# Kernel tuning notes

Hardware: AMD Instinct MI355X
Metric: run time of the kernel (lower is better)

Reference implementation:

```python
import jax, jax.numpy as jnp
import numpy as np

N_EMBD = 1024
N_HEAD = 16
HEAD_SIZE = N_EMBD // N_HEAD


def setup_inputs() -> dict:
    key = jax.random.key(0)
    k1, k2, k3, k4 = jax.random.split(key, 4)
    x = jax.random.normal(k1, (2, 2048, N_EMBD), dtype=jnp.float32)
    # nn.Linear weights: stored as [out, in]; apply as x @ W.T
    scale = 1.0 / np.sqrt(N_EMBD)
    W_kqv = jax.random.uniform(k2, (3 * N_EMBD, N_EMBD), jnp.float32, -scale, scale)
    W_proj = jax.random.uniform(k3, (N_EMBD, N_EMBD), jnp.float32, -scale, scale)
    b_proj = jax.random.uniform(k4, (N_EMBD,), jnp.float32, -scale, scale)
    return {"x": x, "W_kqv": W_kqv, "W_proj": W_proj, "b_proj": b_proj}


def reference(x, W_kqv, W_proj, b_proj):
    B, T, C = x.shape
    H, D = N_HEAD, HEAD_SIZE
    kqv = x @ W_kqv.T  # [B, T, 3C]
    # source splits as k, q, v (k first)
    k, q, v = jnp.split(kqv, 3, axis=-1)
    k = k.reshape(B, T, H, D).transpose(0, 2, 1, 3)  # [B,H,T,D]
    q = q.reshape(B, T, H, D).transpose(0, 2, 1, 3)
    v = v.reshape(B, T, H, D).transpose(0, 2, 1, 3)
    wei = jnp.einsum('bhqd,bhkd->bhqk', q, k) * (D ** -0.5)  # [B,H,T,T]
    causal = jnp.tril(jnp.ones((T, T), dtype=bool))
    wei = jnp.where(causal[None, None], wei, -jnp.inf)
    wei = jax.nn.softmax(wei, axis=-1)
    out = jnp.einsum('bhqk,bhkd->bhqd', wei, v)  # [B,H,T,D]
    out = out.transpose(0, 2, 1, 3).reshape(B, T, C)
    return out @ W_proj.T + b_proj
```

## Files before the change

### kernel.cpp

```cpp
#include <hip/hip_runtime.h>
#include <cstdint>


typedef __bf16 bf16x8 __attribute__((ext_vector_type(8)));
typedef unsigned short u16x8 __attribute__((ext_vector_type(8)));
typedef float f32x4 __attribute__((ext_vector_type(4)));

__device__ __forceinline__ float bf2f(unsigned short u) {
    return __uint_as_float(((unsigned int)u) << 16);
}
__device__ __forceinline__ unsigned short f2bf(float f) {
    unsigned int u = __float_as_uint(f);
    u += 0x7fffu + ((u >> 16) & 1u);
    return (unsigned short)(u >> 16);
}
__device__ __forceinline__ void stC(float* p, float v) { *p = v; }
__device__ __forceinline__ void stC(unsigned short* p, float v) { *p = f2bf(v); }

__device__ __forceinline__ void gl2lds16(const unsigned short* g, unsigned short* l) {
    __builtin_amdgcn_global_load_lds(
        (__attribute__((address_space(1))) void*)g,
        (__attribute__((address_space(3))) void*)l, 16, 0, 0);
}

__device__ __forceinline__ unsigned short* swz(unsigned short* base, int row, int col) {
    const int off = ((row << 7) + (col << 1)) ^ ((row & 7) << 4);
    return (unsigned short*)((char*)base + off);
}
__device__ __forceinline__ const unsigned short* swz(const unsigned short* base, int row, int col) {
    const int off = ((row << 7) + (col << 1)) ^ ((row & 7) << 4);
    return (const unsigned short*)((const char*)base + off);
}

__device__ __forceinline__ void cvt8(const float* __restrict__ s, unsigned short* __restrict__ d) {
    const f32x4 a = *(const f32x4*)s;
    const f32x4 b = *(const f32x4*)(s + 4);
    u16x8 o;
    o[0] = f2bf(a[0]); o[1] = f2bf(a[1]); o[2] = f2bf(a[2]); o[3] = f2bf(a[3]);
    o[4] = f2bf(b[0]); o[5] = f2bf(b[1]); o[6] = f2bf(b[2]); o[7] = f2bf(b[3]);
    *(u16x8*)d = o;
}
__global__ __launch_bounds__(256) void cvt_bf16_3(
    const float* __restrict__ s0, unsigned short* __restrict__ d0, int n0,
    const float* __restrict__ s1, unsigned short* __restrict__ d1, int n1,
    const float* __restrict__ s2, unsigned short* __restrict__ d2, int n2)
{
    const int t = blockIdx.x * 256 + threadIdx.x;
    const int S = gridDim.x * 256;
    for (int i = t; i < n0 / 8; i += S) cvt8(s0 + (size_t)i * 8, d0 + (size_t)i * 8);
    for (int i = t; i < n1 / 8; i += S) cvt8(s1 + (size_t)i * 8, d1 + (size_t)i * 8);
    for (int i = t; i < n2 / 8; i += S) cvt8(s2 + (size_t)i * 8, d2 + (size_t)i * 8);
}

__global__ __launch_bounds__(256, 3) void gemm_qkv(
    const unsigned short* __restrict__ A, const unsigned short* __restrict__ B,
    unsigned short* __restrict__ C, int M, int N, int K)
{
    __shared__ __align__(16) unsigned short As[128 * 32];
    __shared__ __align__(16) unsigned short Bs[128 * 32];

    const int tid = threadIdx.x;
    const int bn = blockIdx.x, bm = blockIdx.y;
    const int w = tid >> 6, lane = tid & 63;
    const int quad = lane >> 4, l16 = lane & 15;
    const int wm = (w >> 1) * 64, wn = (w & 1) * 64;

    f32x4 acc[4][4] = {};

    const int srow = w * 16 + (lane >> 2);
    const int scol = (lane & 3) * 8;
    const unsigned short* Ag = &A[(size_t)(bm * 128 + srow) * K + scol];
    const unsigned short* Bg = &B[(size_t)(bn * 128 + srow) * K + scol];
    unsigned short* AsW = &As[(w * 16) * 32];
    unsigned short* BsW = &Bs[(w * 16) * 32];

    for (int k0 = 0; k0 < K; k0 += 32) {
        gl2lds16(Ag + k0, AsW);
        gl2lds16(Ag + (size_t)64 * K + k0, AsW + 64 * 32);
        gl2lds16(Bg + k0, BsW);
        gl2lds16(Bg + (size_t)64 * K + k0, BsW + 64 * 32);
        __syncthreads();

        bf16x8 af[4], bfr[4];
#pragma unroll
        for (int t = 0; t < 4; t++) {
            af[t]  = *(const bf16x8*)&As[(wm + t * 16 + l16) * 32 + quad * 8];
            bfr[t] = *(const bf16x8*)&Bs[(wn + t * 16 + l16) * 32 + quad * 8];
        }
#pragma unroll
        for (int mt = 0; mt < 4; mt++)
#pragma unroll
            for (int nt = 0; nt < 4; nt++)
                acc[mt][nt] = __builtin_amdgcn_mfma_f32_16x16x32_bf16(
                    af[mt], bfr[nt], acc[mt][nt], 0, 0, 0);
        __syncthreads();
    }

#pragma unroll
    for (int mt = 0; mt < 4; mt++) {
        const int row = bm * 128 + wm + mt * 16 + quad * 4;
#pragma unroll
        for (int nt = 0; nt < 4; nt++) {
            const int col = bn * 128 + wn + nt * 16 + l16;
#pragma unroll
            for (int r = 0; r < 4; r++)
                stC(&C[(size_t)(row + r) * N + col], acc[mt][nt][r]);
        }
    }
}

__global__ __launch_bounds__(256) void gemm_proj(
    const unsigned short* __restrict__ A, const unsigned short* __restrict__ B,
    const float* __restrict__ bias, float* __restrict__ C, int M, int N, int K)
{
    __shared__ __align__(16) unsigned short As[64 * 32];
    __shared__ __align__(16) unsigned short Bs[128 * 32];

    const int tid = threadIdx.x;
    const int bn = blockIdx.x, bm = blockIdx.y;
    const int w = tid >> 6, lane = tid & 63;
    const int quad = lane >> 4, l16 = lane & 15;
    const int wm = (w >> 1) * 32, wn = (w & 1) * 64;

    f32x4 acc[2][4] = {};

    const int srow = w * 16 + (lane >> 2);
    const int scol = (lane & 3) * 8;
    const unsigned short* Ag = &A[(size_t)(bm * 64 + srow) * K + scol];
    const unsigned short* Bg = &B[(size_t)(bn * 128 + srow) * K + scol];
    unsigned short* AsW = &As[(w * 16) * 32];
    unsigned short* BsW = &Bs[(w * 16) * 32];

    for (int k0 = 0; k0 < K; k0 += 32) {
        gl2lds16(Ag + k0, AsW);
        gl2lds16(Bg + k0, BsW);
        gl2lds16(Bg + (size_t)64 * K + k0, BsW + 64 * 32);
        __syncthreads();

        bf16x8 af[2], bfr[4];
#pragma unroll
        for (int t = 0; t < 2; t++)
            af[t]  = *(const bf16x8*)&As[(wm + t * 16 + l16) * 32 + quad * 8];
#pragma unroll
        for (int t = 0; t < 4; t++)
            bfr[t] = *(const bf16x8*)&Bs[(wn + t * 16 + l16) * 32 + quad * 8];
#pragma unroll
        for (int mt = 0; mt < 2; mt++)
#pragma unroll
            for (int nt = 0; nt < 4; nt++)
                acc[mt][nt] = __builtin_amdgcn_mfma_f32_16x16x32_bf16(
                    af[mt], bfr[nt], acc[mt][nt], 0, 0, 0);
        __syncthreads();
    }

#pragma unroll
    for (int mt = 0; mt < 2; mt++) {
        const int row = bm * 64 + wm + mt * 16 + quad * 4;
#pragma unroll
        for (int nt = 0; nt < 4; nt++) {
            const int col = bn * 128 + wn + nt * 16 + l16;
            const float bv = bias[col];
#pragma unroll
            for (int r = 0; r < 4; r++)
                C[(size_t)(row + r) * N + col] = acc[mt][nt][r] + bv;
        }
    }
}

__global__ __launch_bounds__(256) void attn_fused(
    const unsigned short* __restrict__ kqv,
    unsigned short* __restrict__ out)
{
    __shared__ __align__(16) unsigned short Ks[2][64 * 64];
    __shared__ __align__(16) unsigned short Vts[2][64 * 64];
    __shared__ __align__(16) unsigned short Ps[64 * 64];

    const int bh = blockIdx.x;
    const int qt = 31 - (int)blockIdx.y;
    const int b = bh >> 4, h = bh & 15;
    const int tid = threadIdx.x;
    const int w = tid >> 6;
    const int lane = tid & 63;
    const int quad = lane >> 4, l16 = lane & 15;
    const int rowBase = b * 2048;
    const int kOff = h * 64, qOff = 1024 + h * 64, vOff = 2048 + h * 64;
    const float SEXP = 0.125f * 1.4426950408889634f;
    const float MASKV = -1.0e30f;

    bf16x8 aq[2];
    {
        const size_t qrow = (size_t)(rowBase + qt * 64 + w * 16 + l16) * 3072 + qOff;
        aq[0] = *(const bf16x8*)&kqv[qrow + quad * 8];
        aq[1] = *(const bf16x8*)&kqv[qrow + 32 + quad * 8];
    }

    f32x4 o[4] = {};
    float l_i[4] = {0.f, 0.f, 0.f, 0.f};

    u16x8 kr[2], vr[2];
#pragma unroll
    for (int i = 0; i < 2; i++) {
        const int v = tid + i * 256;
        kr[i] = *(const u16x8*)&kqv[(size_t)(rowBase + (v >> 3)) * 3072 + kOff + (v & 7) * 8];
        vr[i] = *(const u16x8*)&kqv[(size_t)(rowBase + lane) * 3072 + vOff + (i * 4 + w) * 8];
    }

    for (int j = 0; j <= qt; j++) {
        const int cur = j & 1;
#pragma unroll
        for (int i = 0; i < 2; i++) {
            const int v = tid + i * 256;
            *(u16x8*)swz(Ks[cur], v >> 3, (v & 7) * 8) = kr[i];
            const int d8 = i * 4 + w;
#pragma unroll
            for (int u = 0; u < 8; u++)
                *swz(Vts[cur], d8 * 8 + u, lane) = vr[i][u];
        }
        __syncthreads();

        if (j < qt) {
#pragma unroll
            for (int i = 0; i < 2; i++) {
                const int v = tid + i * 256;
                kr[i] = *(const u16x8*)&kqv[(size_t)(rowBase + (j + 1) * 64 + (v >> 3)) * 3072 + kOff + (v & 7) * 8];
                vr[i] = *(const u16x8*)&kqv[(size_t)(rowBase + (j + 1) * 64 + lane) * 3072 + vOff + (i * 4 + w) * 8];
            }
        }

        f32x4 s[4] = {};
#pragma unroll
        for (int ks = 0; ks < 2; ks++) {
#pragma unroll
            for (int nt = 0; nt < 4; nt++) {
                const bf16x8 bk = *(const bf16x8*)swz(Ks[cur], nt * 16 + l16, ks * 32 + quad * 8);
                s[nt] = __builtin_amdgcn_mfma_f32_16x16x32_bf16(aq[ks], bk, s[nt], 0, 0, 0);
            }
        }

        if (j == qt) {
            const int rowl = w * 16 + quad * 4;
#pragma unroll
            for (int nt = 0; nt < 4; nt++) {
                const int coll = nt * 16 + l16;
#pragma unroll
                for (int r = 0; r < 4; r++)
                    if (coll > rowl + r) s[nt][r] = MASKV;
            }
        }

#pragma unroll
        for (int nt = 0; nt < 4; nt++) {
#pragma unroll
            for (int r = 0; r < 4; r++) {
                const float p = exp2f(s[nt][r] * SEXP);
                l_i[r] += p;
                *swz(Ps, w * 16 + quad * 4 + r, nt * 16 + l16) = f2bf(p);
            }
        }
        __syncthreads();

#pragma unroll
        for (int ks = 0; ks < 2; ks++) {
            const bf16x8 ap = *(const bf16x8*)swz(Ps, w * 16 + l16, ks * 32 + quad * 8);
#pragma unroll
            for (int nt = 0; nt < 4; nt++) {
                const bf16x8 bv = *(const bf16x8*)swz(Vts[cur], nt * 16 + l16, ks * 32 + quad * 8);
                o[nt] = __builtin_amdgcn_mfma_f32_16x16x32_bf16(ap, bv, o[nt], 0, 0, 0);
            }
        }
    }

    float linv[4];
#pragma unroll
    for (int r = 0; r < 4; r++) {
        float t = l_i[r];
        t += __shfl_xor(t, 1);
        t += __shfl_xor(t, 2);
        t += __shfl_xor(t, 4);
        t += __shfl_xor(t, 8);
        linv[r] = 1.0f / t;
    }

#pragma unroll
    for (int nt = 0; nt < 4; nt++) {
        const int col = h * 64 + nt * 16 + l16;
#pragma unroll
        for (int r = 0; r < 4; r++)
            out[(size_t)(rowBase + qt * 64 + w * 16 + quad * 4 + r) * 1024 + col] =
                f2bf(o[nt][r] * linv[r]);
    }
}

extern "C" void kernel_launch(void* const* d_in, const int* in_sizes, int n_in,
                              void* d_out, int out_size, void* d_ws, size_t ws_size,
                              hipStream_t stream) {
    const float* x     = (const float*)d_in[0];
    const float* Wkqv  = (const float*)d_in[1];
    const float* Wproj = (const float*)d_in[2];
    const float* bproj = (const float*)d_in[3];
    float* out = (float*)d_out;

    unsigned short* kqv    = (unsigned short*)d_ws;
    unsigned short* attn   = kqv    + (size_t)4096 * 3072;
    unsigned short* xb     = attn   + (size_t)4096 * 1024;
    unsigned short* wkqvb  = xb     + (size_t)4096 * 1024;
    unsigned short* wprojb = wkqvb  + (size_t)3072 * 1024;

    cvt_bf16_3<<<dim3(512), dim3(256), 0, stream>>>(
        x, xb, 4096 * 1024, Wkqv, wkqvb, 3072 * 1024, Wproj, wprojb, 1024 * 1024);

    gemm_qkv<<<dim3(24, 32), dim3(256), 0, stream>>>(
        xb, wkqvb, kqv, 4096, 3072, 1024);

    attn_fused<<<dim3(32, 32), dim3(256), 0, stream>>>(kqv, attn);

    gemm_proj<<<dim3(8, 64), dim3(256), 0, stream>>>(
        attn, wprojb, bproj, out, 4096, 1024, 1024);
}
```

Measured before the change: 190.9 us.

## Deepen QKV GEMM K-tile to 64 with XOR-swizzled LDS; stage Q through LDS

The QKV projection GEMM now loads 64-wide K slices per iteration into XOR-swizzled shared memory, halving the number of barrier pairs and doing two MFMA k-steps per load. The attention kernel stages the Q tile through a swizzled LDS buffer with coalesced row loads and rereads Q fragments from LDS each iteration instead of holding them in registers. This aims to cut synchronization overhead and LDS bank conflicts in the GEMM and improve Q load coalescing. The cost is double the GEMM LDS footprint, which may reduce occupancy, plus extra LDS reads per attention tile. The attention Q store to LDS relies on the existing loop barrier before the first read.

```diff
diff --git a/kernel.cpp b/kernel.cpp
--- a/kernel.cpp
+++ b/kernel.cpp
@@ -56,8 +56,8 @@
     const unsigned short* __restrict__ A, const unsigned short* __restrict__ B,
     unsigned short* __restrict__ C, int M, int N, int K)
 {
-    __shared__ __align__(16) unsigned short As[128 * 32];
-    __shared__ __align__(16) unsigned short Bs[128 * 32];
+    __shared__ __align__(16) unsigned short As[128 * 64];
+    __shared__ __align__(16) unsigned short Bs[128 * 64];
 
     const int tid = threadIdx.x;
     const int bn = blockIdx.x, bm = blockIdx.y;
@@ -67,32 +67,36 @@
 
     f32x4 acc[4][4] = {};
 
-    const int srow = w * 16 + (lane >> 2);
-    const int scol = (lane & 3) * 8;
-    const unsigned short* Ag = &A[(size_t)(bm * 128 + srow) * K + scol];
-    const unsigned short* Bg = &B[(size_t)(bn * 128 + srow) * K + scol];
-    unsigned short* AsW = &As[(w * 16) * 32];
-    unsigned short* BsW = &Bs[(w * 16) * 32];
-
-    for (int k0 = 0; k0 < K; k0 += 32) {
-        gl2lds16(Ag + k0, AsW);
-        gl2lds16(Ag + (size_t)64 * K + k0, AsW + 64 * 32);
-        gl2lds16(Bg + k0, BsW);
-        gl2lds16(Bg + (size_t)64 * K + k0, BsW + 64 * 32);
-        __syncthreads();
-
-        bf16x8 af[4], bfr[4];
-#pragma unroll
-        for (int t = 0; t < 4; t++) {
-            af[t]  = *(const bf16x8*)&As[(wm + t * 16 + l16) * 32 + quad * 8];
-            bfr[t] = *(const bf16x8*)&Bs[(wn + t * 16 + l16) * 32 + quad * 8];
-        }
-#pragma unroll
-        for (int mt = 0; mt < 4; mt++)
-#pragma unroll
-            for (int nt = 0; nt < 4; nt++)
-                acc[mt][nt] = __builtin_amdgcn_mfma_f32_16x16x32_bf16(
-                    af[mt], bfr[nt], acc[mt][nt], 0, 0, 0);
+    const int srow = (lane >> 3);
+    const int scol = ((lane & 7) ^ srow) * 8;
+    const unsigned short* Ag = &A[(size_t)(bm * 128 + w * 32 + srow) * K + scol];
+    const unsigned short* Bg = &B[(size_t)(bn * 128 + w * 32 + srow) * K + scol];
+    unsigned short* AsW = &As[(w * 32) * 64];
+    unsigned short* BsW = &Bs[(w * 32) * 64];
+
+    for (int k0 = 0; k0 < K; k0 += 64) {
+#pragma unroll
+        for (int i = 0; i < 4; i++) {
+            gl2lds16(Ag + (size_t)(i * 8) * K + k0, AsW + i * 8 * 64);
+            gl2lds16(Bg + (size_t)(i * 8) * K + k0, BsW + i * 8 * 64);
+        }
+        __syncthreads();
+
+#pragma unroll
+        for (int ks = 0; ks < 2; ks++) {
+            bf16x8 af[4], bfr[4];
+#pragma unroll
+            for (int t = 0; t < 4; t++) {
+                af[t]  = *(const bf16x8*)swz(As, wm + t * 16 + l16, ks * 32 + quad * 8);
+                bfr[t] = *(const bf16x8*)swz(Bs, wn + t * 16 + l16, ks * 32 + quad * 8);
+            }
+#pragma unroll
+            for (int mt = 0; mt < 4; mt++)
+#pragma unroll
+                for (int nt = 0; nt < 4; nt++)
+                    acc[mt][nt] = __builtin_amdgcn_mfma_f32_16x16x32_bf16(
+                        af[mt], bfr[nt], acc[mt][nt], 0, 0, 0);
+        }
         __syncthreads();
     }
 
@@ -171,6 +175,7 @@
     const unsigned short* __restrict__ kqv,
     unsigned short* __restrict__ out)
 {
+    __shared__ __align__(16) unsigned short Qs[64 * 64];
     __shared__ __align__(16) unsigned short Ks[2][64 * 64];
     __shared__ __align__(16) unsigned short Vts[2][64 * 64];
     __shared__ __align__(16) unsigned short Ps[64 * 64];
@@ -187,11 +192,12 @@
     const float SEXP = 0.125f * 1.4426950408889634f;
     const float MASKV = -1.0e30f;
 
-    bf16x8 aq[2];
-    {
-        const size_t qrow = (size_t)(rowBase + qt * 64 + w * 16 + l16) * 3072 + qOff;
-        aq[0] = *(const bf16x8*)&kqv[qrow + quad * 8];
-        aq[1] = *(const bf16x8*)&kqv[qrow + 32 + quad * 8];
+#pragma unroll
+    for (int i = 0; i < 2; i++) {
+        const int v = tid + i * 256;
+        const int row = v >> 3, c8 = (v & 7) * 8;
+        *(u16x8*)swz(Qs, row, c8) =
+            *(const u16x8*)&kqv[(size_t)(rowBase + qt * 64 + row) * 3072 + qOff + c8];
     }
 
     f32x4 o[4] = {};
@@ -230,10 +236,11 @@
         f32x4 s[4] = {};
 #pragma unroll
         for (int ks = 0; ks < 2; ks++) {
+            const bf16x8 aq = *(const bf16x8*)swz(Qs, w * 16 + l16, ks * 32 + quad * 8);
 #pragma unroll
             for (int nt = 0; nt < 4; nt++) {
                 const bf16x8 bk = *(const bf16x8*)swz(Ks[cur], nt * 16 + l16, ks * 32 + quad * 8);
-                s[nt] = __builtin_amdgcn_mfma_f32_16x16x32_bf16(aq[ks], bk, s[nt], 0, 0, 0);
+                s[nt] = __builtin_amdgcn_mfma_f32_16x16x32_bf16(aq, bk, s[nt], 0, 0, 0);
             }
         }
 
```

Measured after the change: 184.5 us. 3.3% less time.
